# Performance work log

Hardware: AMD Instinct MI355X
Metric: run time of the kernel (lower is better)

## Reference

```python
import jax, jax.numpy as jnp
import numpy as np

CHUNK = 128
EPS = 1e-6


def setup_inputs() -> dict:
    key = jax.random.key(0)
    k1, k2, k3 = jax.random.split(key, 3)
    B, H, N, D, E = 4, 8, 4096, 64, 64
    q = jax.random.uniform(k1, (B, H, N, D), dtype=jnp.float32)
    k = jax.random.uniform(k2, (B, H, N, D), dtype=jnp.float32)
    v = jax.random.normal(k3, (B, H, N, E), dtype=jnp.float32)
    return {"q": q, "k": k, "v": v, "inferrring_states": 1}


def reference(q, k, v, inferrring_states):
    # infer_hidden_states path: chunked causal linear attention with carried state.
    B, H, N, D = q.shape
    E = v.shape[-1]
    nc = N // CHUNK
    # [nc, B, H, CHUNK, *] for scan over chunks
    qc = jnp.moveaxis(q.reshape(B, H, nc, CHUNK, D), 2, 0)
    kc = jnp.moveaxis(k.reshape(B, H, nc, CHUNK, D), 2, 0)
    vc = jnp.moveaxis(v.reshape(B, H, nc, CHUNK, E), 2, 0)

    Z0 = jnp.zeros((B, H, 1, D), dtype=q.dtype)        # running sum of k
    S0 = jnp.zeros((B, H, 1, D, E), dtype=q.dtype)     # running sum of k v^T

    def step(carry, qkv):
        Z, S = carry
        qi, ki, vi = qkv
        k_cumsum = Z + jnp.cumsum(ki, axis=-2)                      # [B,H,C,D]
        D_inv = 1.0 / jnp.einsum('bhnd,bhnd->bhn', qi, k_cumsum + EPS)
        context = jnp.einsum('bhnd,bhne->bhnde', ki, vi)            # [B,H,C,D,E]
        ctx_cumsum = S + jnp.cumsum(context, axis=-3)
        out = jnp.einsum('bhnde,bhnd,bhn->bhne', ctx_cumsum, qi, D_inv)
        new_carry = (k_cumsum[:, :, -1:], ctx_cumsum[:, :, -1:])
        return new_carry, out

    (Z, S), outs = jax.lax.scan(step, (Z0, S0), (qc, kc, vc))
    out = jnp.moveaxis(outs, 0, 2).reshape(B, H, N, E)
    # states: Z=[B,H,D], S=[B,H,D,E]
    return out, Z[:, :, 0], S[:, :, 0]
```

## Files before the change

### kernel.cpp

```cpp
#include <hip/hip_runtime.h>


#define CHUNKSZ 128
#define DD 64
#define EE 64
#define NC 32
#define NBH 32
#define NSEQ 4096
#define EPSV 1e-6f
#define OUT0 (NBH * NSEQ * EE)
#define KV_ELEMS (NBH * NC * DD * EE)

typedef short bf16x8 __attribute__((ext_vector_type(8)));
typedef short bf16x4 __attribute__((ext_vector_type(4)));
typedef float f32x4  __attribute__((ext_vector_type(4)));

__device__ __forceinline__ unsigned short f2bf(float f) {
    union { float f; unsigned u; } x; x.f = f;
    unsigned u = x.u + 0x7FFFu + ((x.u >> 16) & 1u);
    return (unsigned short)(u >> 16);
}
__device__ __forceinline__ float bf2f(unsigned short s) {
    union { unsigned u; float f; } x; x.u = ((unsigned)s) << 16;
    return x.f;
}

__global__ __launch_bounds__(256) void la_phase1(
    const float* __restrict__ k, const float* __restrict__ v,
    unsigned short* __restrict__ kvT, float* __restrict__ ks)
{
    const int blk = blockIdx.x;
    const int bh = blk / NC, c = blk % NC;
    const size_t rowbase = (size_t)bh * NSEQ + (size_t)c * CHUNKSZ;

    __shared__ alignas(16) unsigned short kT[CHUNKSZ * DD];
    __shared__ alignas(16) unsigned short vT[CHUNKSZ * EE];
    __shared__ float ksp[4][DD];

    char* kb = (char*)kT;
    char* vb = (char*)vT;

    const int t = threadIdx.x;
    const int w = t >> 6, l = t & 63;
    const int lg = l >> 4, lm = l & 15;
    const int col = t & 63;

    float kpart = 0.f;
#pragma unroll
    for (int pass = 0; pass < 4; ++pass) {
        const int mg = w + 4 * pass;
        const float* kp = k + (rowbase + mg * 8) * DD + col;
        const float* vp = v + (rowbase + mg * 8) * EE + col;
        float kf[8], vf[8];
#pragma unroll
        for (int j = 0; j < 8; ++j) kf[j] = kp[(size_t)j * DD];
#pragma unroll
        for (int j = 0; j < 8; ++j) vf[j] = vp[(size_t)j * EE];
        bf16x8 ku, vu;
#pragma unroll
        for (int j = 0; j < 8; ++j) {
            kpart += kf[j];
            ku[j] = (short)f2bf(kf[j]);
            vu[j] = (short)f2bf(vf[j]);
        }
        *(bf16x8*)(kb + mg * 1024 + col * 16) = ku;
        *(bf16x8*)(vb + mg * 1024 + col * 16) = vu;
    }
    ksp[w][col] = kpart;
    __syncthreads();

    f32x4 acc[4] = {};
#pragma unroll
    for (int kk = 0; kk < 4; ++kk) {
        bf16x8 aK = *(bf16x8*)(kb + (lg + 4 * kk) * 1024 + (16 * w + lm) * 16);
#pragma unroll
        for (int ei = 0; ei < 4; ++ei) {
            bf16x8 bV = *(bf16x8*)(vb + (lg + 4 * kk) * 1024 + (16 * ei + lm) * 16);
            acc[ei] = __builtin_amdgcn_mfma_f32_16x16x32_bf16(aK, bV, acc[ei], 0, 0, 0);
        }
    }
    unsigned short* kvout = kvT + (size_t)(bh * NC + c) * DD * EE;
#pragma unroll
    for (int ei = 0; ei < 4; ++ei) {
        bf16x4 u;
        u[0] = (short)f2bf(acc[ei][0]); u[1] = (short)f2bf(acc[ei][1]);
        u[2] = (short)f2bf(acc[ei][2]); u[3] = (short)f2bf(acc[ei][3]);
        *(bf16x4*)(kvout + (16 * ei + lm) * DD + 16 * w + 4 * lg) = u;
    }
    if (t < DD)
        ks[(size_t)(bh * NC + c) * DD + t] = ksp[0][t] + ksp[1][t] + ksp[2][t] + ksp[3][t];
}

__global__ __launch_bounds__(64) void la_phase2(
    unsigned short* __restrict__ kvT, float* __restrict__ ks, float* __restrict__ out)
{
    const int bid = blockIdx.x, t = threadIdx.x;
    if (bid < 256) {
        const int gid = bid * 64 + t;
        const int bh = gid >> 9;
        const int g = gid & 511;
        unsigned short* base = kvT + (size_t)bh * (NC * DD * EE) + (size_t)g * 8;
        bf16x8 vals[NC];
#pragma unroll
        for (int c = 0; c < NC; ++c)
            vals[c] = *(const bf16x8*)(base + (size_t)c * (DD * EE));
        float run[8] = {};
#pragma unroll
        for (int c = 0; c < NC; ++c) {
            bf16x8 pr;
#pragma unroll
            for (int j = 0; j < 8; ++j) pr[j] = (short)f2bf(run[j]);
            *(bf16x8*)(base + (size_t)c * (DD * EE)) = pr;
#pragma unroll
            for (int j = 0; j < 8; ++j) run[j] += bf2f((unsigned short)vals[c][j]);
        }
        const int e = g >> 3, d0 = (g & 7) * 8;
        float* Sout = out + OUT0 + NBH * DD + (size_t)bh * DD * EE;
#pragma unroll
        for (int j = 0; j < 8; ++j)
            Sout[(size_t)(d0 + j) * EE + e] = run[j];
    } else {
        const int tid = (bid - 256) * 64 + t;
        const int bh = tid >> 6, d = tid & 63;
        float vals[NC];
#pragma unroll
        for (int c = 0; c < NC; ++c)
            vals[c] = ks[(size_t)(bh * NC + c) * DD + d];
        float run = 0.f;
#pragma unroll
        for (int c = 0; c < NC; ++c) {
            float x = vals[c];
            ks[(size_t)(bh * NC + c) * DD + d] = run;
            run += x;
        }
        out[OUT0 + tid] = run;
    }
}

__global__ __launch_bounds__(256) void la_phase3(
    const float* __restrict__ q, const float* __restrict__ k,
    const float* __restrict__ v, const unsigned short* __restrict__ kvT,
    const float* __restrict__ ks, float* __restrict__ out)
{
    const int blk = blockIdx.x;
    const int bh = blk / NC, c = blk % NC;
    const size_t rowbase = (size_t)bh * NSEQ + (size_t)c * CHUNKSZ;

    __shared__ alignas(16) unsigned short k_lds[CHUNKSZ * DD];
    __shared__ alignas(16) unsigned short v_lds[CHUNKSZ * EE];
    __shared__ alignas(16) unsigned short s_lds[CHUNKSZ * CHUNKSZ];
    __shared__ alignas(16) unsigned short st_lds[DD * EE];
    __shared__ float dinv_lds[CHUNKSZ];
    __shared__ float zi_lds[DD];

    char* kb  = (char*)k_lds;
    char* vb  = (char*)v_lds;
    char* sb  = (char*)s_lds;
    char* stb = (char*)st_lds;

    const int t  = threadIdx.x;
    const int w  = t >> 6;
    const int l  = t & 63;
    const int lg = l >> 4;
    const int lm = l & 15;
    const int ni_of[2] = { w, 7 - w };

    {
        bf16x8 z = {0,0,0,0,0,0,0,0};
#pragma unroll
        for (int i = 0; i < 8; ++i)
            *(bf16x8*)(sb + t * 128 + i * 16) = z;
    }
    {
        const float4* kg = (const float4*)(k + rowbase * DD);
#pragma unroll
        for (int i = 0; i < 8; ++i) {
            int idx = t + i * 256;
            int m = idx >> 4, c4 = idx & 15;
            float4 f = kg[idx];
            bf16x4 u;
            u[0] = (short)f2bf(f.x); u[1] = (short)f2bf(f.y);
            u[2] = (short)f2bf(f.z); u[3] = (short)f2bf(f.w);
            int byt = m * 128 + ((c4 * 8) ^ ((m & 7) << 4));
            *(bf16x4*)(kb + byt) = u;
        }
    }
    {
        const int col = t & 63;
#pragma unroll
        for (int pass = 0; pass < 4; ++pass) {
            const int mg = (t >> 6) + 4 * pass;
            const float* vp = v + (rowbase + mg * 8) * EE + col;
            float vf[8];
#pragma unroll
            for (int j = 0; j < 8; ++j) vf[j] = vp[(size_t)j * EE];
            bf16x8 u;
#pragma unroll
            for (int j = 0; j < 8; ++j) u[j] = (short)f2bf(vf[j]);
            *(bf16x8*)(vb + mg * 1024 + col * 16) = u;
        }
    }
    {
        const unsigned short* sg = kvT + (size_t)(bh * NC + c) * DD * EE;
#pragma unroll
        for (int i = 0; i < 2; ++i) {
            int idx = t + 256 * i;
            int e = idx >> 3;
            bf16x8 x = *(const bf16x8*)(sg + (size_t)idx * 8);
            int byt = e * 128 + (((idx & 7) * 16) ^ ((e & 7) << 4));
            *(bf16x8*)(stb + byt) = x;
        }
    }
    if (t < DD) zi_lds[t] = ks[(size_t)(bh * NC + c) * DD + t];

    bf16x8 a_q[2][2];
#pragma unroll
    for (int ni2 = 0; ni2 < 2; ++ni2) {
        int ni = ni_of[ni2];
        const float* qrow = q + (rowbase + 16 * ni + lm) * DD;
#pragma unroll
        for (int kk = 0; kk < 2; ++kk) {
            const float4* p = (const float4*)(qrow + 8 * lg + 32 * kk);
            float4 f0 = p[0], f1 = p[1];
            bf16x8 u;
            u[0] = (short)f2bf(f0.x); u[1] = (short)f2bf(f0.y);
            u[2] = (short)f2bf(f0.z); u[3] = (short)f2bf(f0.w);
            u[4] = (short)f2bf(f1.x); u[5] = (short)f2bf(f1.y);
            u[6] = (short)f2bf(f1.z); u[7] = (short)f2bf(f1.w);
            a_q[ni2][kk] = u;
        }
    }
    __syncthreads();

#pragma unroll
    for (int ni2 = 0; ni2 < 2; ++ni2) {
        const int ni = ni_of[ni2];
        const int n = 16 * ni + lm;
        float rsum = 0.f;
        for (int mi = 0; mi <= ni; ++mi) {
            f32x4 cc = {0.f, 0.f, 0.f, 0.f};
            const int mrow = 16 * mi + lm;
#pragma unroll
            for (int kk = 0; kk < 2; ++kk) {
                int byt = mrow * 128 + (((8 * lg + 32 * kk) * 2) ^ ((mrow & 7) << 4));
                bf16x8 ak = *(bf16x8*)(kb + byt);
                cc = __builtin_amdgcn_mfma_f32_16x16x32_bf16(ak, a_q[ni2][kk], cc, 0, 0, 0);
            }
            const int m0 = 16 * mi + 4 * lg;
            bf16x4 u;
#pragma unroll
            for (int r = 0; r < 4; ++r) {
                float val = (m0 + r <= n) ? cc[r] : 0.f;
                u[r] = (short)f2bf(val);
                rsum += val;
            }
            *(bf16x4*)(sb + n * 256 + ((m0 * 2) ^ ((n & 7) << 4))) = u;
        }
        float qz = 0.f, qs = 0.f;
#pragma unroll
        for (int kk = 0; kk < 2; ++kk) {
#pragma unroll
            for (int i = 0; i < 8; ++i) {
                float qf = bf2f((unsigned short)a_q[ni2][kk][i]);
                qz += qf * zi_lds[8 * lg + 32 * kk + i];
                qs += qf;
            }
        }
        float part = rsum + qz + EPSV * qs;
        part += __shfl_xor(part, 16);
        part += __shfl_xor(part, 32);
        if (lg == 0) dinv_lds[n] = 1.f / part;
    }
    __syncthreads();

    f32x4 acc[2][4];
#pragma unroll
    for (int ni2 = 0; ni2 < 2; ++ni2) {
        const int ni = ni_of[ni2];
        const int kmax = (ni >> 1) + 1;
#pragma unroll
        for (int ei = 0; ei < 4; ++ei) {
            f32x4 cc = {0.f, 0.f, 0.f, 0.f};
            const int e = 16 * ei + lm;
#pragma unroll
            for (int kk = 0; kk < 2; ++kk) {
                int byt = e * 128 + (((8 * lg + 32 * kk) * 2) ^ ((e & 7) << 4));
                bf16x8 bs = *(bf16x8*)(stb + byt);
                cc = __builtin_amdgcn_mfma_f32_16x16x32_bf16(a_q[ni2][kk], bs, cc, 0, 0, 0);
            }
            const int n = 16 * ni + lm;
            for (int kk = 0; kk < kmax; ++kk) {
                int bytA = n * 256 + (((8 * lg + 32 * kk) * 2) ^ ((n & 7) << 4));
                bf16x8 as = *(bf16x8*)(sb + bytA);
                int bytB = (lg + 4 * kk) * 1024 + e * 16;
                bf16x8 bv = *(bf16x8*)(vb + bytB);
                cc = __builtin_amdgcn_mfma_f32_16x16x32_bf16(as, bv, cc, 0, 0, 0);
            }
            acc[ni2][ei] = cc;
        }
    }
    __syncthreads();

#pragma unroll
    for (int ni2 = 0; ni2 < 2; ++ni2) {
        const int nbase = 16 * ni_of[ni2] + 4 * lg;
#pragma unroll
        for (int ei = 0; ei < 4; ++ei) {
            const int e = 16 * ei + lm;
#pragma unroll
            for (int r = 0; r < 4; ++r) {
                int n = nbase + r;
                out[(rowbase + n) * EE + e] = acc[ni2][ei][r] * dinv_lds[n];
            }
        }
    }
}

extern "C" void kernel_launch(void* const* d_in, const int* in_sizes, int n_in,
                              void* d_out, int out_size, void* d_ws, size_t ws_size,
                              hipStream_t stream)
{
    (void)in_sizes; (void)n_in; (void)out_size; (void)ws_size;
    const float* q = (const float*)d_in[0];
    const float* k = (const float*)d_in[1];
    const float* v = (const float*)d_in[2];
    float* out = (float*)d_out;
    unsigned short* kvT = (unsigned short*)d_ws;
    float* ks = (float*)(kvT + KV_ELEMS);

    la_phase1<<<NBH * NC, 256, 0, stream>>>(k, v, kvT, ks);
    la_phase2<<<288, 64, 0, stream>>>(kvT, ks, out);
    la_phase3<<<NBH * NC, 256, 0, stream>>>(q, k, v, kvT, ks, out);
}
```

Baseline: 51.04 us.

## Stage bf16 k/v copies in phase1 and read them directly in phase3

Phase1 now also writes bf16 copies of k (row-major) and v (pre-transposed LDS layout) to workspace. Phase3 reads these bf16 buffers instead of the fp32 k and v inputs. It loads K fragments and the state matrix straight from global into registers, which drops two LDS buffers and the full zeroing of the score tile (only the partial diagonal tail is zeroed now). Both kernels also remap block indices so consecutive physical blocks spread across bh groups. This halves phase3's k/v read traffic and cuts LDS use, at the cost of extra global writes in phase1 and uncached-in-LDS global reads for K.

```diff
diff --git a/kernel.cpp b/kernel.cpp
--- a/kernel.cpp
+++ b/kernel.cpp
@@ -27,10 +27,12 @@
 
 __global__ __launch_bounds__(256) void la_phase1(
     const float* __restrict__ k, const float* __restrict__ v,
-    unsigned short* __restrict__ kvT, float* __restrict__ ks)
+    unsigned short* __restrict__ kvT, float* __restrict__ ks,
+    unsigned short* __restrict__ krel, unsigned short* __restrict__ vrel)
 {
-    const int blk = blockIdx.x;
-    const int bh = blk / NC, c = blk % NC;
+    const int phys = blockIdx.x;
+    const int blk  = (phys & 7) * 128 + (phys >> 3);
+    const int bh = blk >> 5, c = blk & 31;
     const size_t rowbase = (size_t)bh * NSEQ + (size_t)c * CHUNKSZ;
 
     __shared__ alignas(16) unsigned short kT[CHUNKSZ * DD];
@@ -44,6 +46,9 @@
     const int w = t >> 6, l = t & 63;
     const int lg = l >> 4, lm = l & 15;
     const int col = t & 63;
+
+    unsigned short* krc = krel + (size_t)(bh * NC + c) * (CHUNKSZ * DD);
+    unsigned short* vrc = vrel + (size_t)(bh * NC + c) * (CHUNKSZ * EE);
 
     float kpart = 0.f;
 #pragma unroll
@@ -65,6 +70,10 @@
         }
         *(bf16x8*)(kb + mg * 1024 + col * 16) = ku;
         *(bf16x8*)(vb + mg * 1024 + col * 16) = vu;
+#pragma unroll
+        for (int j = 0; j < 8; ++j)
+            krc[(size_t)(mg * 8 + j) * DD + col] = (unsigned short)ku[j];
+        *(bf16x8*)(vrc + mg * 512 + col * 8) = vu;
     }
     ksp[w][col] = kpart;
     __syncthreads();
@@ -138,25 +147,22 @@
 }
 
 __global__ __launch_bounds__(256) void la_phase3(
-    const float* __restrict__ q, const float* __restrict__ k,
-    const float* __restrict__ v, const unsigned short* __restrict__ kvT,
+    const float* __restrict__ q, const unsigned short* __restrict__ krel,
+    const unsigned short* __restrict__ vrel, const unsigned short* __restrict__ kvT,
     const float* __restrict__ ks, float* __restrict__ out)
 {
-    const int blk = blockIdx.x;
-    const int bh = blk / NC, c = blk % NC;
+    const int phys = blockIdx.x;
+    const int blk  = (phys & 7) * 128 + (phys >> 3);
+    const int bh = blk >> 5, c = blk & 31;
     const size_t rowbase = (size_t)bh * NSEQ + (size_t)c * CHUNKSZ;
 
-    __shared__ alignas(16) unsigned short k_lds[CHUNKSZ * DD];
     __shared__ alignas(16) unsigned short v_lds[CHUNKSZ * EE];
     __shared__ alignas(16) unsigned short s_lds[CHUNKSZ * CHUNKSZ];
-    __shared__ alignas(16) unsigned short st_lds[DD * EE];
     __shared__ float dinv_lds[CHUNKSZ];
     __shared__ float zi_lds[DD];
 
-    char* kb  = (char*)k_lds;
-    char* vb  = (char*)v_lds;
-    char* sb  = (char*)s_lds;
-    char* stb = (char*)st_lds;
+    char* vb = (char*)v_lds;
+    char* sb = (char*)s_lds;
 
     const int t  = threadIdx.x;
     const int w  = t >> 6;
@@ -165,53 +171,23 @@
     const int lm = l & 15;
     const int ni_of[2] = { w, 7 - w };
 
-    {
-        bf16x8 z = {0,0,0,0,0,0,0,0};
-#pragma unroll
-        for (int i = 0; i < 8; ++i)
-            *(bf16x8*)(sb + t * 128 + i * 16) = z;
-    }
-    {
-        const float4* kg = (const float4*)(k + rowbase * DD);
-#pragma unroll
-        for (int i = 0; i < 8; ++i) {
-            int idx = t + i * 256;
-            int m = idx >> 4, c4 = idx & 15;
-            float4 f = kg[idx];
-            bf16x4 u;
-            u[0] = (short)f2bf(f.x); u[1] = (short)f2bf(f.y);
-            u[2] = (short)f2bf(f.z); u[3] = (short)f2bf(f.w);
-            int byt = m * 128 + ((c4 * 8) ^ ((m & 7) << 4));
-            *(bf16x4*)(kb + byt) = u;
-        }
-    }
-    {
-        const int col = t & 63;
-#pragma unroll
-        for (int pass = 0; pass < 4; ++pass) {
-            const int mg = (t >> 6) + 4 * pass;
-            const float* vp = v + (rowbase + mg * 8) * EE + col;
-            float vf[8];
-#pragma unroll
-            for (int j = 0; j < 8; ++j) vf[j] = vp[(size_t)j * EE];
-            bf16x8 u;
-#pragma unroll
-            for (int j = 0; j < 8; ++j) u[j] = (short)f2bf(vf[j]);
-            *(bf16x8*)(vb + mg * 1024 + col * 16) = u;
-        }
-    }
-    {
-        const unsigned short* sg = kvT + (size_t)(bh * NC + c) * DD * EE;
-#pragma unroll
-        for (int i = 0; i < 2; ++i) {
-            int idx = t + 256 * i;
-            int e = idx >> 3;
-            bf16x8 x = *(const bf16x8*)(sg + (size_t)idx * 8);
-            int byt = e * 128 + (((idx & 7) * 16) ^ ((e & 7) << 4));
-            *(bf16x8*)(stb + byt) = x;
-        }
+    const unsigned short* krc = krel + (size_t)(bh * NC + c) * (CHUNKSZ * DD);
+    const unsigned short* vrc = vrel + (size_t)(bh * NC + c) * (CHUNKSZ * EE);
+    const unsigned short* stc = kvT + (size_t)(bh * NC + c) * DD * EE;
+
+#pragma unroll
+    for (int i = 0; i < 4; ++i) {
+        int idx = t + 256 * i;
+        *(bf16x8*)(vb + idx * 16) = *(const bf16x8*)(vrc + (size_t)idx * 8);
     }
     if (t < DD) zi_lds[t] = ks[(size_t)(bh * NC + c) * DD + t];
+
+    bf16x8 b_st[4][2];
+#pragma unroll
+    for (int ei = 0; ei < 4; ++ei)
+#pragma unroll
+        for (int kk = 0; kk < 2; ++kk)
+            b_st[ei][kk] = *(const bf16x8*)(stc + (size_t)(16 * ei + lm) * DD + 8 * lg + 32 * kk);
 
     bf16x8 a_q[2][2];
 #pragma unroll
@@ -242,8 +218,7 @@
             const int mrow = 16 * mi + lm;
 #pragma unroll
             for (int kk = 0; kk < 2; ++kk) {
-                int byt = mrow * 128 + (((8 * lg + 32 * kk) * 2) ^ ((mrow & 7) << 4));
-                bf16x8 ak = *(bf16x8*)(kb + byt);
+                bf16x8 ak = *(const bf16x8*)(krc + (size_t)mrow * DD + 8 * lg + 32 * kk);
                 cc = __builtin_amdgcn_mfma_f32_16x16x32_bf16(ak, a_q[ni2][kk], cc, 0, 0, 0);
             }
             const int m0 = 16 * mi + 4 * lg;
@@ -256,6 +231,11 @@
             }
             *(bf16x4*)(sb + n * 256 + ((m0 * 2) ^ ((n & 7) << 4))) = u;
         }
+        if ((ni & 1) == 0) {
+            bf16x4 z4 = {0, 0, 0, 0};
+            const int m0 = 16 * (ni + 1) + 4 * lg;
+            *(bf16x4*)(sb + n * 256 + ((m0 * 2) ^ ((n & 7) << 4))) = z4;
+        }
         float qz = 0.f, qs = 0.f;
 #pragma unroll
         for (int kk = 0; kk < 2; ++kk) {
@@ -283,11 +263,8 @@
             f32x4 cc = {0.f, 0.f, 0.f, 0.f};
             const int e = 16 * ei + lm;
 #pragma unroll
-            for (int kk = 0; kk < 2; ++kk) {
-                int byt = e * 128 + (((8 * lg + 32 * kk) * 2) ^ ((e & 7) << 4));
-                bf16x8 bs = *(bf16x8*)(stb + byt);
-                cc = __builtin_amdgcn_mfma_f32_16x16x32_bf16(a_q[ni2][kk], bs, cc, 0, 0, 0);
-            }
+            for (int kk = 0; kk < 2; ++kk)
+                cc = __builtin_amdgcn_mfma_f32_16x16x32_bf16(a_q[ni2][kk], b_st[ei][kk], cc, 0, 0, 0);
             const int n = 16 * ni + lm;
             for (int kk = 0; kk < kmax; ++kk) {
                 int bytA = n * 256 + (((8 * lg + 32 * kk) * 2) ^ ((n & 7) << 4));
@@ -327,8 +304,10 @@
     float* out = (float*)d_out;
     unsigned short* kvT = (unsigned short*)d_ws;
     float* ks = (float*)(kvT + KV_ELEMS);
-
-    la_phase1<<<NBH * NC, 256, 0, stream>>>(k, v, kvT, ks);
+    unsigned short* krel = (unsigned short*)(ks + NBH * NC * DD);
+    unsigned short* vrel = krel + (size_t)NBH * NSEQ * DD;
+
+    la_phase1<<<NBH * NC, 256, 0, stream>>>(k, v, kvT, ks, krel, vrel);
     la_phase2<<<288, 64, 0, stream>>>(kvT, ks, out);
-    la_phase3<<<NBH * NC, 256, 0, stream>>>(q, k, v, kvT, ks, out);
-}
+    la_phase3<<<NBH * NC, 256, 0, stream>>>(q, krel, vrel, kvT, ks, out);
+}
```

New measurement: 57.49 us. 12.6% more time.
